# Performance work log

Measured on AMD Instinct MI355X. Metric: run time of the kernel, lower is better.

The kernel has to match this reference:

```python
import jax, jax.numpy as jnp
import numpy as np

N_USERS = 100000
N_ITEMS = 200000
N_NODES = N_USERS + N_ITEMS
D = 64
HYPER = 128
NNZ = 4000000
N_LAYERS = 2


def setup_inputs() -> dict:
    key = jax.random.key(0)
    k = jax.random.split(key, 7)
    return {
        "user_emb": jax.random.normal(k[0], (N_USERS, D), dtype=jnp.float32) * 0.1,
        "item_emb": jax.random.normal(k[1], (N_ITEMS, D), dtype=jnp.float32) * 0.1,
        "user_w": jax.random.normal(k[2], (D, HYPER), dtype=jnp.float32) * 0.1,
        "item_w": jax.random.normal(k[3], (D, HYPER), dtype=jnp.float32) * 0.1,
        "adj_vals": jax.random.uniform(k[4], (NNZ,), dtype=jnp.float32),
        "adj_rows": jax.random.randint(k[5], (NNZ,), 0, N_NODES, dtype=jnp.int32),
        "adj_cols": jax.random.randint(k[6], (NNZ,), 0, N_NODES, dtype=jnp.int32),
    }


def reference(user_emb, item_emb, user_w, item_w, adj_vals, adj_rows, adj_cols):
    # Deterministic forward: keep_rate=1.0 (no edge drop), dropout in eval mode.
    n_users = user_emb.shape[0]
    n_nodes = n_users + item_emb.shape[0]

    emb = jnp.concatenate([user_emb, item_emb], axis=0)  # [N, d]
    hyper_uu = user_emb @ user_w  # [n_users, hyper]
    hyper_ii = item_emb @ item_w  # [n_items, hyper]

    h = emb
    hidden_sum = emb
    gcn_hidden = []
    hgnn_hidden = []
    for _ in range(N_LAYERS):
        # sparse adj @ h  via gather + segment_sum
        gcn = jax.ops.segment_sum(adj_vals[:, None] * h[adj_cols], adj_rows,
                                  num_segments=n_nodes)  # [N, d]
        # HGNN: adj @ (adj.T @ x), small [hyper, d] bottleneck
        hu = hyper_uu @ (hyper_uu.T @ h[:n_users])
        hi = hyper_ii @ (hyper_ii.T @ h[n_users:])
        hg = jnp.concatenate([hu, hi], axis=0)
        gcn_hidden.append(gcn)
        hgnn_hidden.append(hg)
        h = gcn + hg
        hidden_sum = hidden_sum + h

    user_out = hidden_sum[:n_users]
    item_out = hidden_sum[n_users:]
    return (user_out, item_out, jnp.stack(gcn_hidden), jnp.stack(hgnn_hidden))
```

## Files before the change

### kernel.cpp

```cpp
#include <hip/hip_runtime.h>

typedef unsigned short u16;
typedef unsigned int u32;
typedef unsigned long long u64;

#define N_USERS 100000
#define N_ITEMS 200000
#define N_NODES 300000
#define D 64
#define HYP 128
#define NNZ 4000000

constexpr long long SZL      = 19200000LL;
constexpr long long OUT_GCN0 = SZL;
constexpr long long OUT_HG0  = 3*SZL;
constexpr long long OUT_PAIR = 4*SZL;
constexpr long long OUT_PART = OUT_PAIR + 8000000LL;
constexpr long long OUT_BIN  = 2*SZL;

#define BSHIFT 10
#define RPB 1024
constexpr int NBKT = (N_NODES + RPB - 1)/RPB;
#define EPB 8192
constexpr int NB_H = (NNZ + EPB - 1)/EPB;

#define S3_CHUNK 512
constexpr int NB_S3U = (N_USERS + S3_CHUNK - 1)/S3_CHUNK;
constexpr int NB_S3I = (N_ITEMS + S3_CHUNK - 1)/S3_CHUNK;
constexpr int NB_S3  = NB_S3U + NB_S3I;
constexpr int UB64   = N_USERS/32;
constexpr int NB_GEMM= N_NODES/32;
constexpr int NB_INIT= 9375;
constexpr int NB_SPMM= N_NODES/4;
constexpr int RG_U   = (NB_S3U + 31)/32;
constexpr int RG_I   = (NB_S3I + 31)/32;

typedef __attribute__((ext_vector_type(8))) short short8;
typedef __attribute__((ext_vector_type(4))) float f32x4;

__device__ __forceinline__ float bf2f(u16 u){ u32 i = ((u32)u) << 16; return __builtin_bit_cast(float, i); }
__device__ __forceinline__ u16 f2bf(float f){
  u32 i = __builtin_bit_cast(u32, f);
  return (u16)((i + 0x7FFFu + ((i >> 16) & 1u)) >> 16);
}

__device__ __forceinline__ void init_body(int t, const float* __restrict__ ue,
                                          const float* __restrict__ ie,
                                          u16* __restrict__ h_bf, float* __restrict__ hsum){
  int base = t*8;
  const float* src = (base < N_USERS*D) ? (ue + base) : (ie + (base - N_USERS*D));
  float4 v0 = *(const float4*)(src);
  float4 v1 = *(const float4*)(src + 4);
  *(float4*)(hsum + base)     = v0;
  *(float4*)(hsum + base + 4) = v1;
  uint4 p;
  p.x = (u32)f2bf(v0.x) | ((u32)f2bf(v0.y)<<16);
  p.y = (u32)f2bf(v0.z) | ((u32)f2bf(v0.w)<<16);
  p.z = (u32)f2bf(v1.x) | ((u32)f2bf(v1.y)<<16);
  p.w = (u32)f2bf(v1.z) | ((u32)f2bf(v1.w)<<16);
  *(uint4*)(h_bf + base) = p;
}

template<int K, int N, bool C32, bool FUSE, bool AF32>
__device__ __forceinline__ void gemm_body(int bid, const void* __restrict__ A0,
                                          const float* __restrict__ Bu,
                                          const float* __restrict__ Bi,
                                          void* __restrict__ Cv,
                                          const float* __restrict__ gcn0,
                                          float* __restrict__ hsum0,
                                          u16* __restrict__ hbf0,
                                          int ublocks, u32* blds){
  bool it = bid >= ublocks;
  int blk = it ? bid - ublocks : bid;
  const float* B = it ? Bi : Bu;
  size_t aoff = it ? (size_t)ublocks*32*K : 0;
  size_t co   = it ? (size_t)ublocks*32*N : 0;

  constexpr int SROW = N + 2;
  constexpr int PAIRS = K*N/2;
  for (int p = threadIdx.x; p < PAIRS; p += 256){
    int k = p/(N/2), c2 = p%(N/2);
    float f0 = B[2*p], f1 = B[2*p+1];
    blds[k*(SROW/2) + c2] = (u32)f2bf(f0) | ((u32)f2bf(f1)<<16);
  }
  __syncthreads();
  const u16* bl = (const u16*)blds;
  int wave = threadIdx.x>>6, lane = threadIdx.x&63, q = lane>>4, lm = lane&15;
  constexpr int NT = N/32;
  int mt = wave>>1, ntb = (wave&1)*NT;
  int r0 = blk*32;
  f32x4 acc[NT];
  #pragma unroll
  for (int nt=0; nt<NT; ++nt) acc[nt] = (f32x4){0.f,0.f,0.f,0.f};
  size_t arow = aoff + (size_t)(r0 + mt*16 + lm)*K + q*8;
  #pragma unroll
  for (int ks = 0; ks < K/32; ++ks){
    short8 a;
    if (AF32){
      const float* af = (const float*)A0 + arow + ks*32;
      float4 f0 = *(const float4*)af;
      float4 f1 = *(const float4*)(af + 4);
      a[0]=(short)f2bf(f0.x); a[1]=(short)f2bf(f0.y);
      a[2]=(short)f2bf(f0.z); a[3]=(short)f2bf(f0.w);
      a[4]=(short)f2bf(f1.x); a[5]=(short)f2bf(f1.y);
      a[6]=(short)f2bf(f1.z); a[7]=(short)f2bf(f1.w);
    } else {
      a = *(const short8*)((const u16*)A0 + arow + ks*32);
    }
    #pragma unroll
    for (int nt = 0; nt < NT; ++nt){
      short8 b;
      #pragma unroll
      for (int j = 0; j < 8; ++j)
        b[j] = (short)bl[(ks*32 + q*8 + j)*SROW + (ntb+nt)*16 + lm];
      acc[nt] = __builtin_amdgcn_mfma_f32_16x16x32_bf16(a, b, acc[nt], 0, 0, 0);
    }
  }
  #pragma unroll
  for (int nt = 0; nt < NT; ++nt)
    #pragma unroll
    for (int r = 0; r < 4; ++r){
      int row = r0 + mt*16 + q*4 + r;
      int col = (ntb+nt)*16 + lm;
      size_t idx = co + (size_t)row*N + col;
      if (C32){
        float hg = acc[nt][r];
        if (FUSE){
          __builtin_nontemporal_store(hg, &((float*)Cv)[idx]);
          float hv = gcn0[idx] + hg;
          hsum0[idx] += hv;
          hbf0[idx] = f2bf(hv);
        } else {
          ((float*)Cv)[idx] = hg;
        }
      } else {
        ((u16*)Cv)[idx] = f2bf(acc[nt][r]);
      }
    }
}

template<int K, int N, bool C32, bool FUSE>
__global__ __launch_bounds__(256) void k_gemm_tall(const u16* __restrict__ A0,
                                                   const float* __restrict__ Bu,
                                                   const float* __restrict__ Bi,
                                                   void* __restrict__ Cv,
                                                   const float* __restrict__ gcn0,
                                                   float* __restrict__ hsum0,
                                                   u16* __restrict__ hbf0,
                                                   int ublocks){
  __shared__ u32 blds[K*(N+2)/2];
  gemm_body<K,N,C32,FUSE,false>((int)blockIdx.x, A0, Bu, Bi, Cv, gcn0, hsum0, hbf0, ublocks, blds);
}

__global__ __launch_bounds__(256) void k_front(const float* __restrict__ ue,
                                               const float* __restrict__ ie,
                                               u16* __restrict__ h_bf,
                                               float* __restrict__ hsum,
                                               const int* __restrict__ rows_,
                                               int* __restrict__ cnt_bb,
                                               const float* __restrict__ user_w,
                                               const float* __restrict__ item_w,
                                               u16* __restrict__ hyper){
  __shared__ u32 shmem[64*(HYP+2)/2];
  int bid = blockIdx.x;
  int tid = threadIdx.x;
  if (bid < NB_H){
    int* hist = (int*)shmem;
    for (int i = tid; i < NBKT; i += 256) hist[i] = 0;
    __syncthreads();
    #pragma unroll
    for (int it = 0; it < 8; ++it){
      int e4 = bid*EPB + it*1024 + tid*4;
      if (e4 < NNZ){
        int4 r4 = *(const int4*)(rows_ + e4);
        atomicAdd(&hist[min(max(r4.x,0),N_NODES-1)>>BSHIFT], 1);
        atomicAdd(&hist[min(max(r4.y,0),N_NODES-1)>>BSHIFT], 1);
        atomicAdd(&hist[min(max(r4.z,0),N_NODES-1)>>BSHIFT], 1);
        atomicAdd(&hist[min(max(r4.w,0),N_NODES-1)>>BSHIFT], 1);
      }
    }
    __syncthreads();
    for (int i = tid; i < NBKT; i += 256) cnt_bb[i*NB_H + bid] = hist[i];
    return;
  }
  if (bid < NB_H + NB_GEMM){
    int gb = bid - NB_H;
    const void* A0 = (gb < UB64) ? (const void*)ue
                                 : (const void*)(ie - (size_t)UB64*32*64);
    gemm_body<64,HYP,false,false,true>(gb, A0, user_w, item_w, hyper,
                                       nullptr, nullptr, nullptr, UB64, shmem);
    return;
  }
  init_body((bid - NB_H - NB_GEMM)*256 + tid, ue, ie, h_bf, hsum);
}

__global__ __launch_bounds__(256) void k_bscan(int* __restrict__ cnt_bb,
                                               int* __restrict__ btot){
  __shared__ int sA[512], sB[512];
  int b = blockIdx.x, tid = threadIdx.x;
  for (int i = tid; i < 512; i += 256) sA[i] = (i < NB_H) ? cnt_bb[b*NB_H + i] : 0;
  __syncthreads();
  int* cur = sA; int* nxt = sB;
  for (int off = 1; off < 512; off <<= 1){
    for (int i = tid; i < 512; i += 256)
      nxt[i] = cur[i] + ((i >= off) ? cur[i-off] : 0);
    __syncthreads();
    int* t = cur; cur = nxt; nxt = t;
  }
  for (int i = tid; i < NB_H; i += 256)
    cnt_bb[b*NB_H + i] = cur[i] - ((i < NB_H) ? 0 : 0) - cnt_bb[b*NB_H + i] + cnt_bb[b*NB_H + i] - cnt_bb[b*NB_H + i];
}

__global__ __launch_bounds__(256) void k_bscan2(int* __restrict__ cnt_bb,
                                                int* __restrict__ btot){
  __shared__ int sA[512], sB[512];
  int b = blockIdx.x, tid = threadIdx.x;
  for (int i = tid; i < 512; i += 256) sA[i] = (i < NB_H) ? cnt_bb[b*NB_H + i] : 0;
  __syncthreads();
  int* cur = sA; int* nxt = sB;
  for (int off = 1; off < 512; off <<= 1){
    for (int i = tid; i < 512; i += 256)
      nxt[i] = cur[i] + ((i >= off) ? cur[i-off] : 0);
    __syncthreads();
    int* t = cur; cur = nxt; nxt = t;
  }
  for (int i = tid; i < NB_H; i += 256){
    int orig = cnt_bb[b*NB_H + i];
    cnt_bb[b*NB_H + i] = cur[i] - orig;
  }
  if (tid == 0) btot[b] = cur[NB_H-1];
}

__global__ __launch_bounds__(256) void k_bbase(const int* __restrict__ btot,
                                               int* __restrict__ bbase){
  __shared__ int sA[512], sB[512];
  int tid = threadIdx.x;
  for (int i = tid; i < 512; i += 256) sA[i] = (i < NBKT) ? btot[i] : 0;
  __syncthreads();
  int* cur = sA; int* nxt = sB;
  for (int off = 1; off < 512; off <<= 1){
    for (int i = tid; i < 512; i += 256)
      nxt[i] = cur[i] + ((i >= off) ? cur[i-off] : 0);
    __syncthreads();
    int* t = cur; cur = nxt; nxt = t;
  }
  for (int i = tid; i <= NBKT; i += 256)
    bbase[i] = (i == 0) ? 0 : cur[i-1];
}

__global__ __launch_bounds__(256) void k_bbin(const int* __restrict__ rows_,
                                              const int* __restrict__ cols_,
                                              const float* __restrict__ vals_,
                                              const int* __restrict__ cnt_bb,
                                              const int* __restrict__ bbase,
                                              int2* __restrict__ bin){
  __shared__ int cur[NBKT];
  int bid = blockIdx.x, tid = threadIdx.x;
  for (int i = tid; i < NBKT; i += 256)
    cur[i] = bbase[i] + cnt_bb[i*NB_H + bid];
  __syncthreads();
  #pragma unroll
  for (int it = 0; it < 8; ++it){
    int e4 = bid*EPB + it*1024 + tid*4;
    if (e4 < NNZ){
      int4 r4 = *(const int4*)(rows_ + e4);
      int4 c4 = *(const int4*)(cols_ + e4);
      float4 v4 = *(const float4*)(vals_ + e4);
      int rr[4] = {r4.x, r4.y, r4.z, r4.w};
      int cc[4] = {c4.x, c4.y, c4.z, c4.w};
      float vv[4] = {v4.x, v4.y, v4.z, v4.w};
      #pragma unroll
      for (int j = 0; j < 4; ++j){
        int r = min(max(rr[j],0), N_NODES-1);
        int c = min(max(cc[j],0), N_NODES-1);
        int pos = atomicAdd(&cur[r >> BSHIFT], 1);
        pos = min(max(pos,0), NNZ-1);
        int pack = ((r & (RPB-1)) << 19) | c;
        u64 pk = (u64)(u32)pack | ((u64)(u32)__float_as_int(vv[j]) << 32);
        __builtin_nontemporal_store(pk, (u64*)&bin[pos]);
      }
    }
  }
}

__global__ __launch_bounds__(256) void k_bfin(const int2* __restrict__ bin,
                                              const int* __restrict__ bbase,
                                              int* __restrict__ rowptr,
                                              int2* __restrict__ pair_s){
  __shared__ int s_hist[RPB];
  __shared__ int sA[RPB], sB[RPB];
  int b = blockIdx.x, tid = threadIdx.x;
  int ebeg = bbase[b], eend = bbase[b+1];
  int base = ebeg;
  for (int i = tid; i < RPB; i += 256) s_hist[i] = 0;
  __syncthreads();
  for (int e = ebeg + tid; e < eend; e += 256){
    int pack = bin[e].x;
    atomicAdd(&s_hist[(pack >> 19) & (RPB-1)], 1);
  }
  __syncthreads();
  for (int i = tid; i < RPB; i += 256) sA[i] = s_hist[i];
  __syncthreads();
  int* cur = sA; int* nxt = sB;
  for (int off = 1; off < RPB; off <<= 1){
    for (int i = tid; i < RPB; i += 256)
      nxt[i] = cur[i] + ((i >= off) ? cur[i-off] : 0);
    __syncthreads();
    int* t = cur; cur = nxt; nxt = t;
  }
  int r0 = b << BSHIFT;
  for (int i = tid; i < RPB; i += 256){
    int v = base + cur[i] - s_hist[i];
    nxt[i] = v;
    if (r0 + i <= N_NODES) rowptr[r0 + i] = v;
  }
  __syncthreads();
  for (int e = ebeg + tid; e < eend; e += 256){
    int2 pv = bin[e];
    int rl = (pv.x >> 19) & (RPB-1);
    int c  = pv.x & 0x7FFFF;
    int pos = atomicAdd(&nxt[rl], 1);
    pos = min(max(pos,0), NNZ-1);
    pair_s[pos] = make_int2(c, pv.y);
  }
}

__device__ __forceinline__ void step3_body(const u16* __restrict__ Hy,
                                           const u16* __restrict__ Hm,
                                           float* __restrict__ outp, int rows, int k0,
                                           u32* __restrict__ lds){
  u32* hyl = lds;
  u32* hml = lds + 32*65;
  const u16* hyl16 = (const u16*)hyl;
  const u16* hml16 = (const u16*)hml;
  int tid = threadIdx.x;
  int wave = tid>>6, lane = tid&63, q = lane>>4, lm = lane&15;
  f32x4 acc[2][4];
  #pragma unroll
  for (int i=0;i<2;i++)
    #pragma unroll
    for (int j=0;j<4;j++) acc[i][j] = (f32x4){0.f,0.f,0.f,0.f};
  for (int kk=0; kk<S3_CHUNK/32; ++kk){
    int kb = k0 + kk*32;
    #pragma unroll
    for (int d0=0; d0<8; ++d0){
      int d = d0*256 + tid;
      int kr = d>>6, c2 = d&63, g = kb+kr;
      hyl[kr*65 + c2] = (g < rows) ? ((const u32*)Hy)[(size_t)g*64 + c2] : 0u;
    }
    #pragma unroll
    for (int d0=0; d0<4; ++d0){
      int d = d0*256 + tid;
      int kr = d>>5, c2 = d&31, g = kb+kr;
      hml[kr*33 + c2] = (g < rows) ? ((const u32*)Hm)[(size_t)g*32 + c2] : 0u;
    }
    __syncthreads();
    short8 a[2], b[4];
    #pragma unroll
    for (int ml=0; ml<2; ++ml)
      #pragma unroll
      for (int j=0;j<8;j++)
        a[ml][j] = (short)hyl16[(q*8+j)*130 + (wave*2+ml)*16 + lm];
    #pragma unroll
    for (int nt=0; nt<4; ++nt)
      #pragma unroll
      for (int j=0;j<8;j++)
        b[nt][j] = (short)hml16[(q*8+j)*66 + nt*16 + lm];
    #pragma unroll
    for (int ml=0; ml<2; ++ml)
      #pragma unroll
      for (int nt=0; nt<4; ++nt)
        acc[ml][nt] = __builtin_amdgcn_mfma_f32_16x16x32_bf16(a[ml], b[nt], acc[ml][nt], 0,0,0);
    __syncthreads();
  }
  #pragma unroll
  for (int ml=0; ml<2; ++ml)
    #pragma unroll
    for (int nt=0; nt<4; ++nt)
      #pragma unroll
      for (int r=0;r<4;r++){
        int m = (wave*2+ml)*16 + q*4 + r;
        int n = nt*16 + lm;
        __builtin_nontemporal_store(acc[ml][nt][r], &outp[m*64 + n]);
      }
}

__global__ __launch_bounds__(256) void k_step3(const u16* __restrict__ hyper,
                                               const u16* __restrict__ h,
                                               float* __restrict__ part){
  __shared__ u32 lds[32*65 + 32*33];
  int bid = blockIdx.x;
  float* outp = part + (size_t)bid*8192;
  if (bid < NB_S3U)
    step3_body(hyper, h, outp, N_USERS, bid*S3_CHUNK, lds);
  else
    step3_body(hyper + (size_t)N_USERS*HYP, h + (size_t)N_USERS*D,
               outp, N_ITEMS, (bid - NB_S3U)*S3_CHUNK, lds);
}

__global__ void k_reduce(const float* __restrict__ part, float* __restrict__ tmp){
  int cb = blockIdx.x & 31;
  int g  = blockIdx.x >> 5;
  int j  = cb*256 + threadIdx.x;
  int b0, b1; float* dst;
  if (g < RG_U){ b0 = g*32;            b1 = min(b0+32, NB_S3U); dst = tmp; }
  else         { b0 = NB_S3U + (g-RG_U)*32; b1 = min(b0+32, NB_S3); dst = tmp + HYP*D; }
  float s = 0.f;
  for (int b = b0; b < b1; ++b) s += part[(size_t)b*8192 + j];
  atomicAdd(&dst[j], s);
}

__global__ __launch_bounds__(256) void k_spmm(const int* __restrict__ rp,
                                              const int2* __restrict__ ps,
                                              const u16* __restrict__ h,
                                              float* __restrict__ gout){
  int r = blockIdx.x*4 + (threadIdx.x>>6);
  int lane = threadIdx.x & 63;
  int beg = rp[r], end = rp[r+1];
  float acc = 0.f;
  for (int base = beg; base < end; base += 64){
    int c = 0; float v = 0.f;
    if (base + lane < end){ int2 pv = ps[base+lane]; c = pv.x; v = __int_as_float(pv.y); }
    int n = end - base; if (n > 64) n = 64;
    for (int e = 0; e < n; e += 8){
      int ce[8]; float ve[8]; float hv[8];
      #pragma unroll
      for (int j = 0; j < 8; ++j){
        ce[j] = __shfl(c, e + j);
        ve[j] = __shfl(v, e + j);
      }
      #pragma unroll
      for (int j = 0; j < 8; ++j)
        hv[j] = bf2f(h[(size_t)ce[j]*64 + lane]);
      #pragma unroll
      for (int j = 0; j < 8; ++j)
        acc += ve[j] * hv[j];
    }
  }
  gout[(size_t)r*64 + lane] = acc;
}

extern "C" void kernel_launch(void* const* d_in, const int* in_sizes, int n_in,
                              void* d_out, int out_size, void* d_ws, size_t ws_size,
                              hipStream_t stream) {
  const float* user_emb = (const float*)d_in[0];
  const float* item_emb = (const float*)d_in[1];
  const float* user_w   = (const float*)d_in[2];
  const float* item_w   = (const float*)d_in[3];
  const float* adj_vals = (const float*)d_in[4];
  const int* adj_rows = (const int*)d_in[5];
  const int* adj_cols = (const int*)d_in[6];
  float* out = (float*)d_out;

  char* w = (char*)d_ws;
  auto alloc = [&](size_t b){ void* p = (void*)w; w += (b + 255) & ~(size_t)255; return p; };
  u16*   hyper  = (u16*)  alloc((size_t)N_NODES*HYP*2);
  u16*   h_bf   = (u16*)  alloc((size_t)N_NODES*D*2);
  int*   rowptr = (int*)  alloc((size_t)(N_NODES+1)*4);
  int*   cnt_bb = (int*)  alloc((size_t)NBKT*NB_H*4);
  int*   btot   = (int*)  alloc((size_t)NBKT*4);
  int*   bbase  = (int*)  alloc((size_t)(NBKT+1)*4);
  float* tmp_u  = (float*)alloc((size_t)HYP*D*4);
  float* tmp_i  = (float*)alloc((size_t)HYP*D*4);
  (void)tmp_i;

  int2*  pair_s = (int2*)(out + OUT_PAIR);
  float* part   = out + OUT_PART;
  int2*  bin    = (int2*)(out + OUT_BIN);
  float* hsum   = out;

  hipMemsetAsync(tmp_u, 0, (size_t)2*HYP*D*4, stream);

  k_front<<<NB_H + NB_GEMM + NB_INIT, 256, 0, stream>>>(
      user_emb, item_emb, h_bf, hsum, adj_rows, cnt_bb, user_w, item_w, hyper);

  k_bscan2<<<NBKT, 256, 0, stream>>>(cnt_bb, btot);
  k_bbase<<<1, 256, 0, stream>>>(btot, bbase);
  k_bbin<<<NB_H, 256, 0, stream>>>(adj_rows, adj_cols, adj_vals, cnt_bb, bbase, bin);
  k_bfin<<<NBKT, 256, 0, stream>>>(bin, bbase, rowptr, pair_s);

  k_spmm<<<NB_SPMM, 256, 0, stream>>>(rowptr, pair_s, h_bf, out + OUT_GCN0);
  k_step3<<<NB_S3, 256, 0, stream>>>(hyper, h_bf, part);
  k_reduce<<<32*(RG_U+RG_I), 256, 0, stream>>>(part, tmp_u);
  k_gemm_tall<128,64,true,true><<<NB_GEMM, 256, 0, stream>>>(
      hyper, tmp_u, tmp_u + HYP*D, out + OUT_HG0, out + OUT_GCN0, hsum, h_bf, UB64);

  hipMemsetAsync(tmp_u, 0, (size_t)2*HYP*D*4, stream);
  k_spmm<<<NB_SPMM, 256, 0, stream>>>(rowptr, pair_s, h_bf, out + OUT_GCN0 + SZL);
  k_step3<<<NB_S3, 256, 0, stream>>>(hyper, h_bf, part);
  k_reduce<<<32*(RG_U+RG_I), 256, 0, stream>>>(part, tmp_u);
  k_gemm_tall<128,64,true,true><<<NB_GEMM, 256, 0, stream>>>(
      hyper, tmp_u, tmp_u + HYP*D, out + OUT_HG0 + SZL, out + OUT_GCN0 + SZL,
      hsum, h_bf, UB64);
}
```

Baseline: 1.023 ms.

## Fuse step3 into binning kernel and fold partial reduction into SpMM launch

The layer-0 hypergraph partial products (step3) now run in the same launch as the edge-binning pass, and the partial-sum reduction becomes extra blocks of the SpMM launch. The reduction writes its sums directly instead of using atomics, so both memsets go away. The SpMM also switches to nontemporal loads and stores for edge pairs and outputs. This removes several kernel launches and lets independent work overlap, at the cost of 64 serial reduction blocks with long loops that may leave the SpMM tail unbalanced.

```diff
diff --git a/kernel.cpp b/kernel.cpp
--- a/kernel.cpp
+++ b/kernel.cpp
@@ -32,8 +32,7 @@
 constexpr int NB_GEMM= N_NODES/32;
 constexpr int NB_INIT= 9375;
 constexpr int NB_SPMM= N_NODES/4;
-constexpr int RG_U   = (NB_S3U + 31)/32;
-constexpr int RG_I   = (NB_S3I + 31)/32;
+constexpr int NB_RED = 64;
 
 typedef __attribute__((ext_vector_type(8))) short short8;
 typedef __attribute__((ext_vector_type(4))) float f32x4;
@@ -194,11 +193,14 @@
   init_body((bid - NB_H - NB_GEMM)*256 + tid, ue, ie, h_bf, hsum);
 }
 
-__global__ __launch_bounds__(256) void k_bscan(int* __restrict__ cnt_bb,
-                                               int* __restrict__ btot){
-  __shared__ int sA[512], sB[512];
+__global__ __launch_bounds__(256) void k_bscan2(int* __restrict__ cnt_bb,
+                                                int* __restrict__ btot){
+  __shared__ int sO[512], sA[512], sB[512];
   int b = blockIdx.x, tid = threadIdx.x;
-  for (int i = tid; i < 512; i += 256) sA[i] = (i < NB_H) ? cnt_bb[b*NB_H + i] : 0;
+  for (int i = tid; i < 512; i += 256){
+    int v = (i < NB_H) ? cnt_bb[b*NB_H + i] : 0;
+    sO[i] = v; sA[i] = v;
+  }
   __syncthreads();
   int* cur = sA; int* nxt = sB;
   for (int off = 1; off < 512; off <<= 1){
@@ -208,26 +210,7 @@
     int* t = cur; cur = nxt; nxt = t;
   }
   for (int i = tid; i < NB_H; i += 256)
-    cnt_bb[b*NB_H + i] = cur[i] - ((i < NB_H) ? 0 : 0) - cnt_bb[b*NB_H + i] + cnt_bb[b*NB_H + i] - cnt_bb[b*NB_H + i];
-}
-
-__global__ __launch_bounds__(256) void k_bscan2(int* __restrict__ cnt_bb,
-                                                int* __restrict__ btot){
-  __shared__ int sA[512], sB[512];
-  int b = blockIdx.x, tid = threadIdx.x;
-  for (int i = tid; i < 512; i += 256) sA[i] = (i < NB_H) ? cnt_bb[b*NB_H + i] : 0;
-  __syncthreads();
-  int* cur = sA; int* nxt = sB;
-  for (int off = 1; off < 512; off <<= 1){
-    for (int i = tid; i < 512; i += 256)
-      nxt[i] = cur[i] + ((i >= off) ? cur[i-off] : 0);
-    __syncthreads();
-    int* t = cur; cur = nxt; nxt = t;
-  }
-  for (int i = tid; i < NB_H; i += 256){
-    int orig = cnt_bb[b*NB_H + i];
-    cnt_bb[b*NB_H + i] = cur[i] - orig;
-  }
+    cnt_bb[b*NB_H + i] = cur[i] - sO[i];
   if (tid == 0) btot[b] = cur[NB_H-1];
 }
 
@@ -246,83 +229,6 @@
   }
   for (int i = tid; i <= NBKT; i += 256)
     bbase[i] = (i == 0) ? 0 : cur[i-1];
-}
-
-__global__ __launch_bounds__(256) void k_bbin(const int* __restrict__ rows_,
-                                              const int* __restrict__ cols_,
-                                              const float* __restrict__ vals_,
-                                              const int* __restrict__ cnt_bb,
-                                              const int* __restrict__ bbase,
-                                              int2* __restrict__ bin){
-  __shared__ int cur[NBKT];
-  int bid = blockIdx.x, tid = threadIdx.x;
-  for (int i = tid; i < NBKT; i += 256)
-    cur[i] = bbase[i] + cnt_bb[i*NB_H + bid];
-  __syncthreads();
-  #pragma unroll
-  for (int it = 0; it < 8; ++it){
-    int e4 = bid*EPB + it*1024 + tid*4;
-    if (e4 < NNZ){
-      int4 r4 = *(const int4*)(rows_ + e4);
-      int4 c4 = *(const int4*)(cols_ + e4);
-      float4 v4 = *(const float4*)(vals_ + e4);
-      int rr[4] = {r4.x, r4.y, r4.z, r4.w};
-      int cc[4] = {c4.x, c4.y, c4.z, c4.w};
-      float vv[4] = {v4.x, v4.y, v4.z, v4.w};
-      #pragma unroll
-      for (int j = 0; j < 4; ++j){
-        int r = min(max(rr[j],0), N_NODES-1);
-        int c = min(max(cc[j],0), N_NODES-1);
-        int pos = atomicAdd(&cur[r >> BSHIFT], 1);
-        pos = min(max(pos,0), NNZ-1);
-        int pack = ((r & (RPB-1)) << 19) | c;
-        u64 pk = (u64)(u32)pack | ((u64)(u32)__float_as_int(vv[j]) << 32);
-        __builtin_nontemporal_store(pk, (u64*)&bin[pos]);
-      }
-    }
-  }
-}
-
-__global__ __launch_bounds__(256) void k_bfin(const int2* __restrict__ bin,
-                                              const int* __restrict__ bbase,
-                                              int* __restrict__ rowptr,
-                                              int2* __restrict__ pair_s){
-  __shared__ int s_hist[RPB];
-  __shared__ int sA[RPB], sB[RPB];
-  int b = blockIdx.x, tid = threadIdx.x;
-  int ebeg = bbase[b], eend = bbase[b+1];
-  int base = ebeg;
-  for (int i = tid; i < RPB; i += 256) s_hist[i] = 0;
-  __syncthreads();
-  for (int e = ebeg + tid; e < eend; e += 256){
-    int pack = bin[e].x;
-    atomicAdd(&s_hist[(pack >> 19) & (RPB-1)], 1);
-  }
-  __syncthreads();
-  for (int i = tid; i < RPB; i += 256) sA[i] = s_hist[i];
-  __syncthreads();
-  int* cur = sA; int* nxt = sB;
-  for (int off = 1; off < RPB; off <<= 1){
-    for (int i = tid; i < RPB; i += 256)
-      nxt[i] = cur[i] + ((i >= off) ? cur[i-off] : 0);
-    __syncthreads();
-    int* t = cur; cur = nxt; nxt = t;
-  }
-  int r0 = b << BSHIFT;
-  for (int i = tid; i < RPB; i += 256){
-    int v = base + cur[i] - s_hist[i];
-    nxt[i] = v;
-    if (r0 + i <= N_NODES) rowptr[r0 + i] = v;
-  }
-  __syncthreads();
-  for (int e = ebeg + tid; e < eend; e += 256){
-    int2 pv = bin[e];
-    int rl = (pv.x >> 19) & (RPB-1);
-    int c  = pv.x & 0x7FFFF;
-    int pos = atomicAdd(&nxt[rl], 1);
-    pos = min(max(pos,0), NNZ-1);
-    pair_s[pos] = make_int2(c, pv.y);
-  }
 }
 
 __device__ __forceinline__ void step3_body(const u16* __restrict__ Hy,
@@ -385,11 +291,9 @@
       }
 }
 
-__global__ __launch_bounds__(256) void k_step3(const u16* __restrict__ hyper,
+__device__ __forceinline__ void step3_dispatch(int bid, const u16* __restrict__ hyper,
                                                const u16* __restrict__ h,
-                                               float* __restrict__ part){
-  __shared__ u32 lds[32*65 + 32*33];
-  int bid = blockIdx.x;
+                                               float* __restrict__ part, u32* lds){
   float* outp = part + (size_t)bid*8192;
   if (bid < NB_S3U)
     step3_body(hyper, h, outp, N_USERS, bid*S3_CHUNK, lds);
@@ -398,29 +302,127 @@
                outp, N_ITEMS, (bid - NB_S3U)*S3_CHUNK, lds);
 }
 
-__global__ void k_reduce(const float* __restrict__ part, float* __restrict__ tmp){
-  int cb = blockIdx.x & 31;
-  int g  = blockIdx.x >> 5;
-  int j  = cb*256 + threadIdx.x;
-  int b0, b1; float* dst;
-  if (g < RG_U){ b0 = g*32;            b1 = min(b0+32, NB_S3U); dst = tmp; }
-  else         { b0 = NB_S3U + (g-RG_U)*32; b1 = min(b0+32, NB_S3); dst = tmp + HYP*D; }
-  float s = 0.f;
-  for (int b = b0; b < b1; ++b) s += part[(size_t)b*8192 + j];
-  atomicAdd(&dst[j], s);
+__global__ __launch_bounds__(256) void k_step3(const u16* __restrict__ hyper,
+                                               const u16* __restrict__ h,
+                                               float* __restrict__ part){
+  __shared__ u32 lds[32*65 + 32*33];
+  step3_dispatch((int)blockIdx.x, hyper, h, part, lds);
+}
+
+__global__ __launch_bounds__(256) void k_mid(const int* __restrict__ rows_,
+                                             const int* __restrict__ cols_,
+                                             const float* __restrict__ vals_,
+                                             const int* __restrict__ cnt_bb,
+                                             const int* __restrict__ bbase,
+                                             int2* __restrict__ bin,
+                                             const u16* __restrict__ hyper,
+                                             const u16* __restrict__ h_bf,
+                                             float* __restrict__ part){
+  __shared__ u32 lds[32*65 + 32*33];
+  int bid = blockIdx.x, tid = threadIdx.x;
+  if (bid < NB_H){
+    int* cur = (int*)lds;
+    for (int i = tid; i < NBKT; i += 256)
+      cur[i] = bbase[i] + cnt_bb[i*NB_H + bid];
+    __syncthreads();
+    #pragma unroll
+    for (int it = 0; it < 8; ++it){
+      int e4 = bid*EPB + it*1024 + tid*4;
+      if (e4 < NNZ){
+        int4 r4 = *(const int4*)(rows_ + e4);
+        int4 c4 = *(const int4*)(cols_ + e4);
+        float4 v4 = *(const float4*)(vals_ + e4);
+        int rr[4] = {r4.x, r4.y, r4.z, r4.w};
+        int cc[4] = {c4.x, c4.y, c4.z, c4.w};
+        float vv[4] = {v4.x, v4.y, v4.z, v4.w};
+        #pragma unroll
+        for (int j = 0; j < 4; ++j){
+          int r = min(max(rr[j],0), N_NODES-1);
+          int c = min(max(cc[j],0), N_NODES-1);
+          int pos = atomicAdd(&cur[r >> BSHIFT], 1);
+          pos = min(max(pos,0), NNZ-1);
+          int pack = ((r & (RPB-1)) << 19) | c;
+          u64 pk = (u64)(u32)pack | ((u64)(u32)__float_as_int(vv[j]) << 32);
+          __builtin_nontemporal_store(pk, (u64*)&bin[pos]);
+        }
+      }
+    }
+    return;
+  }
+  step3_dispatch(bid - NB_H, hyper, h_bf, part, lds);
+}
+
+__global__ __launch_bounds__(256) void k_bfin(const int2* __restrict__ bin,
+                                              const int* __restrict__ bbase,
+                                              int* __restrict__ rowptr,
+                                              int2* __restrict__ pair_s){
+  __shared__ int s_hist[RPB];
+  __shared__ int sA[RPB], sB[RPB];
+  int b = blockIdx.x, tid = threadIdx.x;
+  int ebeg = bbase[b], eend = bbase[b+1];
+  int base = ebeg;
+  for (int i = tid; i < RPB; i += 256) s_hist[i] = 0;
+  __syncthreads();
+  for (int e = ebeg + tid; e < eend; e += 256){
+    int pack = bin[e].x;
+    atomicAdd(&s_hist[(pack >> 19) & (RPB-1)], 1);
+  }
+  __syncthreads();
+  for (int i = tid; i < RPB; i += 256) sA[i] = s_hist[i];
+  __syncthreads();
+  int* cur = sA; int* nxt = sB;
+  for (int off = 1; off < RPB; off <<= 1){
+    for (int i = tid; i < RPB; i += 256)
+      nxt[i] = cur[i] + ((i >= off) ? cur[i-off] : 0);
+    __syncthreads();
+    int* t = cur; cur = nxt; nxt = t;
+  }
+  int r0 = b << BSHIFT;
+  for (int i = tid; i < RPB; i += 256){
+    int v = base + cur[i] - s_hist[i];
+    nxt[i] = v;
+    if (r0 + i <= N_NODES) rowptr[r0 + i] = v;
+  }
+  __syncthreads();
+  for (int e = ebeg + tid; e < eend; e += 256){
+    int2 pv = bin[e];
+    int rl = (pv.x >> 19) & (RPB-1);
+    int c  = pv.x & 0x7FFFF;
+    int pos = atomicAdd(&nxt[rl], 1);
+    pos = min(max(pos,0), NNZ-1);
+    pair_s[pos] = make_int2(c, pv.y);
+  }
 }
 
 __global__ __launch_bounds__(256) void k_spmm(const int* __restrict__ rp,
                                               const int2* __restrict__ ps,
                                               const u16* __restrict__ h,
-                                              float* __restrict__ gout){
-  int r = blockIdx.x*4 + (threadIdx.x>>6);
+                                              float* __restrict__ gout,
+                                              const float* __restrict__ part,
+                                              float* __restrict__ tmp){
+  int bid = blockIdx.x;
+  if (bid < NB_RED){
+    int j = (bid & 31)*256 + threadIdx.x;
+    float s = 0.f;
+    if (bid < 32){
+      for (int b = 0; b < NB_S3U; ++b) s += part[(size_t)b*8192 + j];
+      tmp[j] = s;
+    } else {
+      for (int b = NB_S3U; b < NB_S3; ++b) s += part[(size_t)b*8192 + j];
+      tmp[HYP*D + j] = s;
+    }
+    return;
+  }
+  int r = (bid - NB_RED)*4 + (threadIdx.x>>6);
   int lane = threadIdx.x & 63;
   int beg = rp[r], end = rp[r+1];
   float acc = 0.f;
   for (int base = beg; base < end; base += 64){
     int c = 0; float v = 0.f;
-    if (base + lane < end){ int2 pv = ps[base+lane]; c = pv.x; v = __int_as_float(pv.y); }
+    if (base + lane < end){
+      u64 pvu = __builtin_nontemporal_load((const u64*)(ps + base + lane));
+      c = (int)(u32)pvu; v = __int_as_float((int)(u32)(pvu >> 32));
+    }
     int n = end - base; if (n > 64) n = 64;
     for (int e = 0; e < n; e += 8){
       int ce[8]; float ve[8]; float hv[8];
@@ -437,7 +439,7 @@
         acc += ve[j] * hv[j];
     }
   }
-  gout[(size_t)r*64 + lane] = acc;
+  __builtin_nontemporal_store(acc, &gout[(size_t)r*64 + lane]);
 }
 
 extern "C" void kernel_launch(void* const* d_in, const int* in_sizes, int n_in,
@@ -469,26 +471,25 @@
   int2*  bin    = (int2*)(out + OUT_BIN);
   float* hsum   = out;
 
-  hipMemsetAsync(tmp_u, 0, (size_t)2*HYP*D*4, stream);
-
   k_front<<<NB_H + NB_GEMM + NB_INIT, 256, 0, stream>>>(
       user_emb, item_emb, h_bf, hsum, adj_rows, cnt_bb, user_w, item_w, hyper);
 
   k_bscan2<<<NBKT, 256, 0, stream>>>(cnt_bb, btot);
   k_bbase<<<1, 256, 0, stream>>>(btot, bbase);
-  k_bbin<<<NB_H, 256, 0, stream>>>(adj_rows, adj_cols, adj_vals, cnt_bb, bbase, bin);
+
+  k_mid<<<NB_H + NB_S3, 256, 0, stream>>>(adj_rows, adj_cols, adj_vals,
+                                          cnt_bb, bbase, bin, hyper, h_bf, part);
+
   k_bfin<<<NBKT, 256, 0, stream>>>(bin, bbase, rowptr, pair_s);
 
-  k_spmm<<<NB_SPMM, 256, 0, stream>>>(rowptr, pair_s, h_bf, out + OUT_GCN0);
-  k_step3<<<NB_S3, 256, 0, stream>>>(hyper, h_bf, part);
-  k_reduce<<<32*(RG_U+RG_I), 256, 0, stream>>>(part, tmp_u);
+  k_spmm<<<NB_RED + NB_SPMM, 256, 0, stream>>>(rowptr, pair_s, h_bf,
+                                               out + OUT_GCN0, part, tmp_u);
   k_gemm_tall<128,64,true,true><<<NB_GEMM, 256, 0, stream>>>(
       hyper, tmp_u, tmp_u + HYP*D, out + OUT_HG0, out + OUT_GCN0, hsum, h_bf, UB64);
 
-  hipMemsetAsync(tmp_u, 0, (size_t)2*HYP*D*4, stream);
-  k_spmm<<<NB_SPMM, 256, 0, stream>>>(rowptr, pair_s, h_bf, out + OUT_GCN0 + SZL);
   k_step3<<<NB_S3, 256, 0, stream>>>(hyper, h_bf, part);
-  k_reduce<<<32*(RG_U+RG_I), 256, 0, stream>>>(part, tmp_u);
+  k_spmm<<<NB_RED + NB_SPMM, 256, 0, stream>>>(rowptr, pair_s, h_bf,
+                                               out + OUT_GCN0 + SZL, part, tmp_u);
   k_gemm_tall<128,64,true,true><<<NB_GEMM, 256, 0, stream>>>(
       hyper, tmp_u, tmp_u + HYP*D, out + OUT_HG0 + SZL, out + OUT_GCN0 + SZL,
       hsum, h_bf, UB64);
```

After: 997.1 us. -2.5%, faster.
